# Performance work log

Hardware: AMD Instinct MI355X
Metric: run time of the kernel (lower is better)

The kernel has to match this reference:

```python
import jax, jax.numpy as jnp
import numpy as np

B, T, D, EXP, K = 4, 2048, 1024, 2, 4
H = D * EXP


def setup_inputs() -> dict:
    key = jax.random.key(0)
    ks = jax.random.split(key, 8)
    x = jax.random.normal(ks[0], (B, T, D), jnp.float32)
    W_in = jax.random.normal(ks[1], (2 * H, D), jnp.float32) * D ** -0.5
    s_conv = 1.0 / np.sqrt(K)  # fan_in = (in_ch/groups)*K = K
    W_conv = jax.random.uniform(ks[2], (H, 1, K), jnp.float32, -s_conv, s_conv)
    b_conv = jax.random.uniform(ks[3], (H,), jnp.float32, -s_conv, s_conv)
    W_gates = jax.random.normal(ks[4], (3 * H, H), jnp.float32) * H ** -0.5
    s_g = 1.0 / np.sqrt(H)
    b_gates = jax.random.uniform(ks[5], (3 * H,), jnp.float32, -s_g, s_g)
    W_out = jax.random.normal(ks[6], (D, H), jnp.float32) * H ** -0.5
    alpha_p = jnp.asarray(1.0, jnp.float32)
    return {"x": x, "W_in": W_in, "W_conv": W_conv, "b_conv": b_conv,
            "W_gates": W_gates, "b_gates": b_gates, "W_out": W_out,
            "alpha_p": alpha_p}


def _scan_combine(c1, c2):
    a1, b1 = c1
    a2, b2 = c2
    return (a1 * a2, a2 * b1 + b2)


def reference(x, W_in, W_conv, b_conv, W_gates, b_gates, W_out, alpha_p):
    # input projection -> gate branch and conv branch, each [B,T,H]
    gi = jnp.einsum('btd,ed->bte', x, W_in)
    gate, u = jnp.split(gi, 2, axis=-1)
    # causal depthwise conv over time (torch pads K-1 both sides then keeps [:T])
    uc = jnp.transpose(u, (0, 2, 1))  # [B,H,T]
    v = jax.lax.conv_general_dilated(
        uc, W_conv, window_strides=(1,), padding=[(K - 1, 0)],
        dimension_numbers=('NCH', 'OIH', 'NCH'), feature_group_count=H)
    v = jnp.transpose(v + b_conv[None, :, None], (0, 2, 1))  # [B,T,H]
    # gates
    g = jnp.einsum('bth,gh->btg', v, W_gates) + b_gates
    f, i, o = jnp.split(g, 3, axis=-1)
    # reversed_sigmoid=True: alpha = sigmoid(-f) ** relu(alpha_p)
    alpha = jax.nn.sigmoid(-f) ** jax.nn.relu(alpha_p)
    xin = jax.nn.sigmoid(i) * v
    # diagonal linear recurrence h_t = alpha_t * h_{t-1} + xin_t via parallel scan
    _, h = jax.lax.associative_scan(_scan_combine, (alpha, xin), axis=1)
    h = jax.nn.sigmoid(o) * h
    return jnp.einsum('bth,dh->btd', jax.nn.gelu(gate, approximate=False) * h, W_out)
```

## Files before the change

kernel.cpp:

```cpp
#include <hip/hip_runtime.h>
#include <hip/hip_bf16.h>
#include <cstdint>
#include <cstddef>

#define B_ 4
#define T_ 2048
#define D_ 1024
#define H_ 2048

typedef __attribute__((ext_vector_type(8))) short s8v;
typedef __attribute__((ext_vector_type(4))) float f4v;

__device__ __forceinline__ float bflo(unsigned int u){ union{unsigned int i;float f;}c; c.i=u<<16; return c.f; }
__device__ __forceinline__ float bfhi(unsigned int u){ union{unsigned int i;float f;}c; c.i=u&0xffff0000u; return c.f; }
__device__ __forceinline__ unsigned short f2bf(float f){
    __hip_bfloat16 h = __float2bfloat16(f);
    union { __hip_bfloat16 h; unsigned short u; } c; c.h = h; return c.u;
}
__device__ __forceinline__ unsigned int pk2(float lo, float hi){
    return (unsigned int)f2bf(lo) | ((unsigned int)f2bf(hi) << 16);
}
__device__ __forceinline__ float sigm(float x){ return 1.f/(1.f+expf(-x)); }

__device__ __forceinline__ void gload16(const void* g, void* l){
    __builtin_amdgcn_global_load_lds(
        (const __attribute__((address_space(1))) unsigned int*)g,
        (__attribute__((address_space(3))) unsigned int*)l, 16, 0, 0);
}

__global__ __launch_bounds__(256)
void cvt8(const float* __restrict__ s, unsigned short* __restrict__ d)
{
    size_t i = ((size_t)blockIdx.x*256 + threadIdx.x)*8;
    float4 a = *(const float4*)(s+i), b = *(const float4*)(s+i+4);
    uint4 o; o.x=pk2(a.x,a.y); o.y=pk2(a.z,a.w); o.z=pk2(b.x,b.y); o.w=pk2(b.z,b.w);
    *(uint4*)(d+i)=o;
}

template<int AM, int BM, int EPI>
__global__ __launch_bounds__(256)
void mgemm(const void* __restrict__ Asrc, int lda,
           const void* __restrict__ Bsrc, int K, int N,
           const float* __restrict__ bias,
           unsigned short* __restrict__ C0, unsigned short* __restrict__ C1,
           unsigned short* __restrict__ C2, float* __restrict__ Cf,
           const unsigned short* __restrict__ vsrc, const float* __restrict__ app)
{
    __shared__ unsigned short As[128*64];
    __shared__ unsigned short Bs[128*64];
    const int tid = threadIdx.x;
    const int lane = tid & 63;
    const int wid = tid >> 6;

    const int nwg = gridDim.x * 64;
    const int orig = blockIdx.y * gridDim.x + blockIdx.x;
    const int q = nwg >> 3;
    const int wg = (orig & 7) * q + (orig >> 3);
    const int m0 = (wg & 63) * 128;
    const int n0 = (wg >> 6) * 128;

    const int ar0 = wid * 32;
    const int alr = lane >> 3;
    const int alj = lane & 7;
    const int rr = tid >> 1;
    const int kh = tid & 1;

    const int wm = wid >> 1, wn = wid & 1;
    const int fr = lane & 15, fg = lane >> 4;
    int aoff[4][2], boff[4][2];
#pragma unroll
    for (int m = 0; m < 4; ++m) {
        int row = wm*64 + m*16 + fr;
#pragma unroll
        for (int s = 0; s < 2; ++s)
            aoff[m][s] = row*128 + (((s*4 + fg) ^ (row & 7)) * 16);
    }
#pragma unroll
    for (int n = 0; n < 4; ++n) {
        int row = wn*64 + n*16 + fr;
#pragma unroll
        for (int s = 0; s < 2; ++s)
            boff[n][s] = row*128 + (((s*4 + fg) ^ (row & 7)) * 16);
    }
    const char* Asc = (const char*)As;
    const char* Bsc = (const char*)Bs;

    f4v acc[4][4];
#pragma unroll
    for (int m = 0; m < 4; ++m)
#pragma unroll
        for (int n = 0; n < 4; ++n) { f4v z4 = {0.f,0.f,0.f,0.f}; acc[m][n] = z4; }

    for (int k0 = 0; k0 < K; k0 += 64) {
        if (AM == 1) {
            const unsigned short* Ab = (const unsigned short*)Asrc;
#pragma unroll
            for (int i = 0; i < 4; ++i) {
                int row = ar0 + i*8 + alr;
                int ss = alj ^ alr;
                const char* g = (const char*)(Ab + (size_t)(m0+row)*lda + k0) + ss*16;
                gload16(g, (void*)((char*)As + (ar0 + i*8)*128));
            }
        } else {
            const float* src = (const float*)Asrc + (size_t)(m0+rr)*lda + k0 + kh*32;
            float4 v[8];
#pragma unroll
            for (int i = 0; i < 8; ++i) v[i] = ((const float4*)src)[i];
#pragma unroll
            for (int qd = 0; qd < 4; ++qd) {
                uint4 w;
                w.x = pk2(v[2*qd].x, v[2*qd].y);   w.y = pk2(v[2*qd].z, v[2*qd].w);
                w.z = pk2(v[2*qd+1].x, v[2*qd+1].y); w.w = pk2(v[2*qd+1].z, v[2*qd+1].w);
                int j = (kh*4 + qd) ^ (rr & 7);
                *(uint4*)((char*)As + rr*128 + j*16) = w;
            }
        }
        if (BM == 1) {
            const unsigned short* Bb = (const unsigned short*)Bsrc;
#pragma unroll
            for (int i = 0; i < 4; ++i) {
                int row = ar0 + i*8 + alr;
                int ss = alj ^ alr;
                const char* g = (const char*)(Bb + (size_t)(n0+row)*K + k0) + ss*16;
                gload16(g, (void*)((char*)Bs + (ar0 + i*8)*128));
            }
        } else {
            const float* src = (const float*)Bsrc + (size_t)(n0+rr)*K + k0 + kh*32;
            float4 v[8];
#pragma unroll
            for (int i = 0; i < 8; ++i) v[i] = ((const float4*)src)[i];
#pragma unroll
            for (int qd = 0; qd < 4; ++qd) {
                uint4 w;
                w.x = pk2(v[2*qd].x, v[2*qd].y);   w.y = pk2(v[2*qd].z, v[2*qd].w);
                w.z = pk2(v[2*qd+1].x, v[2*qd+1].y); w.w = pk2(v[2*qd+1].z, v[2*qd+1].w);
                int j = (kh*4 + qd) ^ (rr & 7);
                *(uint4*)((char*)Bs + rr*128 + j*16) = w;
            }
        }
        __syncthreads();
#pragma unroll
        for (int s = 0; s < 2; ++s) {
            s8v a[4], b[4];
#pragma unroll
            for (int m = 0; m < 4; ++m) a[m] = *(const s8v*)(Asc + aoff[m][s]);
#pragma unroll
            for (int n = 0; n < 4; ++n) b[n] = *(const s8v*)(Bsc + boff[n][s]);
#pragma unroll
            for (int m = 0; m < 4; ++m)
#pragma unroll
                for (int n = 0; n < 4; ++n)
                    acc[m][n] = __builtin_amdgcn_mfma_f32_16x16x32_bf16(a[m], b[n], acc[m][n], 0, 0, 0);
        }
        __syncthreads();
    }

    float apv = 1.f; bool ap1 = true;
    if (EPI == 2) { apv = fmaxf(app[0], 0.f); ap1 = (apv == 1.0f); }
    const int cr = (lane >> 4) * 4;
    const int cc = lane & 15;
#pragma unroll
    for (int m = 0; m < 4; ++m) {
        const int grow0 = m0 + wm*64 + m*16 + cr;
#pragma unroll
        for (int n = 0; n < 4; ++n) {
            const int colb = n0 + wn*64 + n*16;
            const int gcol = colb + cc;
            if (EPI == 0) {
#pragma unroll
                for (int j = 0; j < 4; ++j)
                    Cf[(size_t)(grow0+j)*N + gcol] = acc[m][n][j];
            } else if (EPI == 1) {
                unsigned short* dst = (colb < H_) ? C0 : C1;
                const int pc = gcol & (H_-1);
#pragma unroll
                for (int j = 0; j < 4; ++j)
                    dst[(size_t)(grow0+j)*H_ + pc] = f2bf(acc[m][n][j]);
            } else {
                const int plane = colb >> 11;
                const int pc = gcol & (H_-1);
#pragma unroll
                for (int j = 0; j < 4; ++j) {
                    float val = acc[m][n][j] + bias[gcol];
                    const size_t off = (size_t)(grow0+j)*H_ + pc;
                    if (plane == 0) {
                        float s = 1.f/(1.f+expf(val));
                        C0[off] = f2bf(ap1 ? s : powf(s, apv));
                    } else if (plane == 1) {
                        C1[off] = f2bf(sigm(val) * bflo(vsrc[off]));
                    } else {
                        C2[off] = f2bf(sigm(val));
                    }
                }
            }
        }
    }
}

__global__ __launch_bounds__(256)
void conv8(const unsigned short* __restrict__ u, const float* __restrict__ Wc,
           const float* __restrict__ bc, unsigned short* __restrict__ v)
{
    size_t i8 = ((size_t)blockIdx.x*256 + threadIdx.x) * 8;
    int h = (int)(i8 % H_);
    size_t bt = i8 / H_;
    int t = (int)(bt % T_);
    float w[8][4], acc[8];
#pragma unroll
    for (int j = 0; j < 8; ++j) {
        float4 wr = *(const float4*)(Wc + (h+j)*4);
        w[j][0]=wr.x; w[j][1]=wr.y; w[j][2]=wr.z; w[j][3]=wr.w;
        acc[j] = bc[h+j];
    }
    const unsigned short* up = u + bt*H_ + h;
#pragma unroll
    for (int k = 0; k < 4; ++k) {
        int dt = 3 - k;
        if (t >= dt) {
            uint4 r = *(const uint4*)(up - (size_t)dt*H_);
            float e[8] = {bflo(r.x),bfhi(r.x),bflo(r.y),bfhi(r.y),
                          bflo(r.z),bfhi(r.z),bflo(r.w),bfhi(r.w)};
#pragma unroll
            for (int j = 0; j < 8; ++j) acc[j] = fmaf(e[j], w[j][k], acc[j]);
        }
    }
    uint4 o;
    o.x = pk2(acc[0],acc[1]); o.y = pk2(acc[2],acc[3]);
    o.z = pk2(acc[4],acc[5]); o.w = pk2(acc[6],acc[7]);
    *(uint4*)(v + i8) = o;
}

__global__ __launch_bounds__(256)
void scan_chunk8(const unsigned short* __restrict__ al, const unsigned short* __restrict__ xi,
                 float* __restrict__ cA, float* __restrict__ cB, int CT)
{
    int hh = threadIdx.x * 8;
    int c = blockIdx.y, b = blockIdx.z;
    size_t base = ((size_t)b*T_ + (size_t)c*CT)*H_ + hh;
    float A[8], Bv[8];
#pragma unroll
    for (int j=0;j<8;++j){ A[j]=1.f; Bv[j]=0.f; }
    for (int t = 0; t < CT; ++t) {
        uint4 wa = *(const uint4*)(al+base);
        uint4 wx = *(const uint4*)(xi+base);
        float a[8]={bflo(wa.x),bfhi(wa.x),bflo(wa.y),bfhi(wa.y),bflo(wa.z),bfhi(wa.z),bflo(wa.w),bfhi(wa.w)};
        float x[8]={bflo(wx.x),bfhi(wx.x),bflo(wx.y),bfhi(wx.y),bflo(wx.z),bfhi(wx.z),bflo(wx.w),bfhi(wx.w)};
#pragma unroll
        for (int j=0;j<8;++j){ A[j]*=a[j]; Bv[j]=fmaf(a[j],Bv[j],x[j]); }
        base += H_;
    }
    size_t ci = ((size_t)b*gridDim.y + c)*H_ + hh;
    *(float4*)(cA+ci)   = (float4){A[0],A[1],A[2],A[3]};
    *(float4*)(cA+ci+4) = (float4){A[4],A[5],A[6],A[7]};
    *(float4*)(cB+ci)   = (float4){Bv[0],Bv[1],Bv[2],Bv[3]};
    *(float4*)(cB+ci+4) = (float4){Bv[4],Bv[5],Bv[6],Bv[7]};
}

__global__ __launch_bounds__(256)
void scan_carry8(const float* __restrict__ cA, const float* __restrict__ cB,
                 float* __restrict__ cin, int NC)
{
    int gt = blockIdx.x*256 + threadIdx.x;
    int hh = (gt * 8) % H_;
    int b  = (gt * 8) / H_;
    float h[8];
#pragma unroll
    for (int j=0;j<8;++j) h[j]=0.f;
    for (int c = 0; c < NC; ++c) {
        size_t ci = ((size_t)b*NC + c)*H_ + hh;
        *(float4*)(cin+ci)   = (float4){h[0],h[1],h[2],h[3]};
        *(float4*)(cin+ci+4) = (float4){h[4],h[5],h[6],h[7]};
        float4 a0 = *(const float4*)(cA+ci), a1 = *(const float4*)(cA+ci+4);
        float4 b0 = *(const float4*)(cB+ci), b1 = *(const float4*)(cB+ci+4);
        float a[8]={a0.x,a0.y,a0.z,a0.w,a1.x,a1.y,a1.z,a1.w};
        float x[8]={b0.x,b0.y,b0.z,b0.w,b1.x,b1.y,b1.z,b1.w};
#pragma unroll
        for (int j=0;j<8;++j) h[j] = fmaf(a[j], h[j], x[j]);
    }
}

__global__ __launch_bounds__(256)
void scan_apply8(const unsigned short* __restrict__ al, const unsigned short* __restrict__ xi,
                 const unsigned short* __restrict__ so, const unsigned short* __restrict__ ga,
                 const float* __restrict__ cin, unsigned short* __restrict__ z, int CT)
{
    int hh = threadIdx.x * 8;
    int c = blockIdx.y, b = blockIdx.z;
    size_t base = ((size_t)b*T_ + (size_t)c*CT)*H_ + hh;
    size_t ci = ((size_t)b*gridDim.y + c)*H_ + hh;
    float h[8];
    {
        float4 h0 = *(const float4*)(cin+ci), h1 = *(const float4*)(cin+ci+4);
        h[0]=h0.x; h[1]=h0.y; h[2]=h0.z; h[3]=h0.w;
        h[4]=h1.x; h[5]=h1.y; h[6]=h1.z; h[7]=h1.w;
    }
    for (int t = 0; t < CT; ++t) {
        uint4 wa = *(const uint4*)(al+base);
        uint4 wx = *(const uint4*)(xi+base);
        uint4 ws_ = *(const uint4*)(so+base);
        uint4 wg = *(const uint4*)(ga+base);
        float a[8]={bflo(wa.x),bfhi(wa.x),bflo(wa.y),bfhi(wa.y),bflo(wa.z),bfhi(wa.z),bflo(wa.w),bfhi(wa.w)};
        float x[8]={bflo(wx.x),bfhi(wx.x),bflo(wx.y),bfhi(wx.y),bflo(wx.z),bfhi(wx.z),bflo(wx.w),bfhi(wx.w)};
        float s[8]={bflo(ws_.x),bfhi(ws_.x),bflo(ws_.y),bfhi(ws_.y),bflo(ws_.z),bfhi(ws_.z),bflo(ws_.w),bfhi(ws_.w)};
        float g[8]={bflo(wg.x),bfhi(wg.x),bflo(wg.y),bfhi(wg.y),bflo(wg.z),bfhi(wg.z),bflo(wg.w),bfhi(wg.w)};
        float zo[8];
#pragma unroll
        for (int j=0;j<8;++j) {
            h[j] = fmaf(a[j], h[j], x[j]);
            float ge = 0.5f*g[j]*(1.f+erff(g[j]*0.70710678118654752f));
            zo[j] = ge * s[j] * h[j];
        }
        uint4 o;
        o.x = pk2(zo[0],zo[1]); o.y = pk2(zo[2],zo[3]);
        o.z = pk2(zo[4],zo[5]); o.w = pk2(zo[6],zo[7]);
        *(uint4*)(z + base) = o;
        base += H_;
    }
}

__global__ void zero_out(float* __restrict__ out, size_t n)
{
    for (size_t i = (size_t)blockIdx.x*256 + threadIdx.x; i < n; i += (size_t)gridDim.x*256)
        out[i] = 0.f;
}

extern "C" void kernel_launch(void* const* d_in, const int* in_sizes, int n_in,
                              void* d_out, int out_size, void* d_ws, size_t ws_size,
                              hipStream_t stream)
{
    const float* x       = (const float*)d_in[0];
    const float* W_in    = (const float*)d_in[1];
    const float* W_conv  = (const float*)d_in[2];
    const float* b_conv  = (const float*)d_in[3];
    const float* W_gates = (const float*)d_in[4];
    const float* b_gates = (const float*)d_in[5];
    const float* W_out   = (const float*)d_in[6];
    const float* alpha_p = (const float*)d_in[7];
    float* out = (float*)d_out;

    const size_t plane = (size_t)B_ * T_ * H_;
    unsigned short* gate = (unsigned short*)d_ws;
    unsigned short* u    = gate + plane;
    unsigned short* v    = u + plane;
    unsigned short* xin  = v + plane;
    unsigned short* so   = xin + plane;
    char* R = (char*)(so + plane);

    const size_t x_elems  = (size_t)B_*T_*D_;
    const size_t wg_elems = (size_t)3*H_*H_;
    const size_t wi_elems = (size_t)2*H_*D_;
    const size_t wo_elems = (size_t)D_*H_;
    const int NCF = 64;
    const size_t carry_b = 3*(size_t)B_*NCF*H_*4;
    const size_t Rneed = x_elems*2 > carry_b + wo_elems*2 ? x_elems*2 : carry_b + wo_elems*2;
    const size_t need_fast = 5*plane*2 + Rneed;

    if (ws_size >= need_fast && (size_t)out_size*4 >= (wg_elems + wi_elems)*2) {
        unsigned short* wgb  = (unsigned short*)d_out;
        unsigned short* winb = wgb + wg_elems;
        unsigned short* xb   = (unsigned short*)R;
        float* cAp  = (float*)R;
        float* cBp  = cAp + (size_t)B_*NCF*H_;
        float* cinp = cBp + (size_t)B_*NCF*H_;
        unsigned short* woutb = (unsigned short*)(cinp + (size_t)B_*NCF*H_);
        const int CT = T_ / NCF;

        cvt8<<<(unsigned)(x_elems/2048),  256, 0, stream>>>(x, xb);
        cvt8<<<(unsigned)(wi_elems/2048), 256, 0, stream>>>(W_in, winb);
        cvt8<<<(unsigned)(wg_elems/2048), 256, 0, stream>>>(W_gates, wgb);
        mgemm<1,1,1><<<dim3(32,64), 256, 0, stream>>>(
            xb, D_, winb, D_, 2*H_, nullptr, gate, u, nullptr, nullptr, nullptr, nullptr);
        conv8<<<(unsigned)(plane/8/256), 256, 0, stream>>>(u, W_conv, b_conv, v);
        cvt8<<<(unsigned)(wo_elems/2048), 256, 0, stream>>>(W_out, woutb);
        mgemm<1,1,2><<<dim3(48,64), 256, 0, stream>>>(
            v, H_, wgb, H_, 3*H_, b_gates, u, xin, so, nullptr, v, alpha_p);
        scan_chunk8<<<dim3(1,NCF,B_), 256, 0, stream>>>(u, xin, cAp, cBp, CT);
        scan_carry8<<<(B_*H_/8)/256, 256, 0, stream>>>(cAp, cBp, cinp, NCF);
        scan_apply8<<<dim3(1,NCF,B_), 256, 0, stream>>>(u, xin, so, gate, cinp, v, CT);
        mgemm<1,1,0><<<dim3(8,64), 256, 0, stream>>>(
            v, H_, woutb, H_, D_, nullptr, nullptr, nullptr, nullptr, out, nullptr, nullptr);
        return;
    }

    float* cAp = (float*)R;
    int NC = 64;
    if (ws_size < 5*plane*2 + 3*(size_t)B_*64*H_*4) {
        NC = 16;
        if (ws_size < 5*plane*2 + 3*(size_t)B_*16*H_*4) {
            zero_out<<<2048, 256, 0, stream>>>(out, (size_t)out_size);
            return;
        }
    }
    const int CT = T_ / NC;
    float* cBp  = cAp + (size_t)B_*NC*H_;
    float* cinp = cBp + (size_t)B_*NC*H_;

    mgemm<0,0,1><<<dim3(32,64), 256, 0, stream>>>(
        x, D_, W_in, D_, 2*H_, nullptr, gate, u, nullptr, nullptr, nullptr, nullptr);
    conv8<<<(unsigned)(plane/8/256), 256, 0, stream>>>(u, W_conv, b_conv, v);
    mgemm<1,0,2><<<dim3(48,64), 256, 0, stream>>>(
        v, H_, W_gates, H_, 3*H_, b_gates, u, xin, so, nullptr, v, alpha_p);
    scan_chunk8<<<dim3(1,NC,B_), 256, 0, stream>>>(u, xin, cAp, cBp, CT);
    scan_carry8<<<(B_*H_/8)/256, 256, 0, stream>>>(cAp, cBp, cinp, NC);
    scan_apply8<<<dim3(1,NC,B_), 256, 0, stream>>>(u, xin, so, gate, cinp, v, CT);
    mgemm<1,0,0><<<dim3(8,64), 256, 0, stream>>>(
        v, H_, W_out, H_, D_, nullptr, nullptr, nullptr, nullptr, out, nullptr, nullptr);
}
```

Measured before the change: 647.7 us.

## Add 256x256 double-buffered GEMM kernel for input and gate projections

Adds a new GEMM kernel that uses 256x256 output tiles with 512 threads (8 waves, each computing 128x64). It double-buffers LDS and issues the next K-tile's global-to-LDS loads between MFMA phases, raising MFMA priority with s_setprio. The input-projection and gate GEMMs now use it, aiming for more data reuse per loaded byte and overlap of loads with compute. The cost is 128KB of LDS and large accumulator register use, which lowers occupancy, and far fewer workgroups (512 and 768), which may fill the CUs unevenly.

```diff
diff --git a/kernel.cpp b/kernel.cpp
--- a/kernel.cpp
+++ b/kernel.cpp
@@ -37,120 +37,111 @@
     *(uint4*)(d+i)=o;
 }
 
-template<int AM, int BM, int EPI>
-__global__ __launch_bounds__(256)
-void mgemm(const void* __restrict__ Asrc, int lda,
-           const void* __restrict__ Bsrc, int K, int N,
-           const float* __restrict__ bias,
-           unsigned short* __restrict__ C0, unsigned short* __restrict__ C1,
-           unsigned short* __restrict__ C2, float* __restrict__ Cf,
-           const unsigned short* __restrict__ vsrc, const float* __restrict__ app)
-{
-    __shared__ unsigned short As[128*64];
-    __shared__ unsigned short Bs[128*64];
+template<int EPI>
+__global__ __launch_bounds__(512)
+void mgemm256(const unsigned short* __restrict__ A, int lda,
+              const unsigned short* __restrict__ Bw, int K, int N,
+              const float* __restrict__ bias,
+              unsigned short* __restrict__ C0, unsigned short* __restrict__ C1,
+              unsigned short* __restrict__ C2,
+              const unsigned short* __restrict__ vsrc, const float* __restrict__ app)
+{
+    __shared__ unsigned short As[2][256*64];
+    __shared__ unsigned short Bs[2][256*64];
     const int tid = threadIdx.x;
     const int lane = tid & 63;
     const int wid = tid >> 6;
-
-    const int nwg = gridDim.x * 64;
-    const int orig = blockIdx.y * gridDim.x + blockIdx.x;
+    const int wm = wid >> 2;
+    const int wn = wid & 3;
+
+    const int nxb = N >> 8;
+    const int nwg = nxb * 32;
+    const int orig = blockIdx.x;
     const int q = nwg >> 3;
     const int wg = (orig & 7) * q + (orig >> 3);
-    const int m0 = (wg & 63) * 128;
-    const int n0 = (wg >> 6) * 128;
-
-    const int ar0 = wid * 32;
-    const int alr = lane >> 3;
-    const int alj = lane & 7;
-    const int rr = tid >> 1;
-    const int kh = tid & 1;
-
-    const int wm = wid >> 1, wn = wid & 1;
+    const int m0 = (wg & 31) * 256;
+    const int n0 = (wg >> 5) * 256;
+
+    const int srow_in8 = lane >> 3;
+    const int sslot    = (lane & 7) ^ srow_in8;
+    const int NT = K >> 6;
+
     const int fr = lane & 15, fg = lane >> 4;
-    int aoff[4][2], boff[4][2];
-#pragma unroll
-    for (int m = 0; m < 4; ++m) {
-        int row = wm*64 + m*16 + fr;
+    const int sw = fr & 7;
+    int aoff[8][2], boff[4][2];
+#pragma unroll
+    for (int m = 0; m < 8; ++m) {
+        int row = wm*128 + m*16 + fr;
 #pragma unroll
         for (int s = 0; s < 2; ++s)
-            aoff[m][s] = row*128 + (((s*4 + fg) ^ (row & 7)) * 16);
+            aoff[m][s] = row*128 + (((s*4 + fg) ^ sw) * 16);
     }
 #pragma unroll
     for (int n = 0; n < 4; ++n) {
         int row = wn*64 + n*16 + fr;
 #pragma unroll
         for (int s = 0; s < 2; ++s)
-            boff[n][s] = row*128 + (((s*4 + fg) ^ (row & 7)) * 16);
-    }
-    const char* Asc = (const char*)As;
-    const char* Bsc = (const char*)Bs;
-
-    f4v acc[4][4];
-#pragma unroll
-    for (int m = 0; m < 4; ++m)
+            boff[n][s] = row*128 + (((s*4 + fg) ^ sw) * 16);
+    }
+
+    f4v acc[8][4];
+#pragma unroll
+    for (int m = 0; m < 8; ++m)
 #pragma unroll
         for (int n = 0; n < 4; ++n) { f4v z4 = {0.f,0.f,0.f,0.f}; acc[m][n] = z4; }
 
-    for (int k0 = 0; k0 < K; k0 += 64) {
-        if (AM == 1) {
-            const unsigned short* Ab = (const unsigned short*)Asrc;
-#pragma unroll
-            for (int i = 0; i < 4; ++i) {
-                int row = ar0 + i*8 + alr;
-                int ss = alj ^ alr;
-                const char* g = (const char*)(Ab + (size_t)(m0+row)*lda + k0) + ss*16;
-                gload16(g, (void*)((char*)As + (ar0 + i*8)*128));
-            }
-        } else {
-            const float* src = (const float*)Asrc + (size_t)(m0+rr)*lda + k0 + kh*32;
-            float4 v[8];
-#pragma unroll
-            for (int i = 0; i < 8; ++i) v[i] = ((const float4*)src)[i];
-#pragma unroll
-            for (int qd = 0; qd < 4; ++qd) {
-                uint4 w;
-                w.x = pk2(v[2*qd].x, v[2*qd].y);   w.y = pk2(v[2*qd].z, v[2*qd].w);
-                w.z = pk2(v[2*qd+1].x, v[2*qd+1].y); w.w = pk2(v[2*qd+1].z, v[2*qd+1].w);
-                int j = (kh*4 + qd) ^ (rr & 7);
-                *(uint4*)((char*)As + rr*128 + j*16) = w;
-            }
-        }
-        if (BM == 1) {
-            const unsigned short* Bb = (const unsigned short*)Bsrc;
-#pragma unroll
-            for (int i = 0; i < 4; ++i) {
-                int row = ar0 + i*8 + alr;
-                int ss = alj ^ alr;
-                const char* g = (const char*)(Bb + (size_t)(n0+row)*K + k0) + ss*16;
-                gload16(g, (void*)((char*)Bs + (ar0 + i*8)*128));
-            }
-        } else {
-            const float* src = (const float*)Bsrc + (size_t)(n0+rr)*K + k0 + kh*32;
-            float4 v[8];
-#pragma unroll
-            for (int i = 0; i < 8; ++i) v[i] = ((const float4*)src)[i];
-#pragma unroll
-            for (int qd = 0; qd < 4; ++qd) {
-                uint4 w;
-                w.x = pk2(v[2*qd].x, v[2*qd].y);   w.y = pk2(v[2*qd].z, v[2*qd].w);
-                w.z = pk2(v[2*qd+1].x, v[2*qd+1].y); w.w = pk2(v[2*qd+1].z, v[2*qd+1].w);
-                int j = (kh*4 + qd) ^ (rr & 7);
-                *(uint4*)((char*)Bs + rr*128 + j*16) = w;
-            }
-        }
-        __syncthreads();
-#pragma unroll
-        for (int s = 0; s < 2; ++s) {
-            s8v a[4], b[4];
-#pragma unroll
-            for (int m = 0; m < 4; ++m) a[m] = *(const s8v*)(Asc + aoff[m][s]);
-#pragma unroll
-            for (int n = 0; n < 4; ++n) b[n] = *(const s8v*)(Bsc + boff[n][s]);
-#pragma unroll
-            for (int m = 0; m < 4; ++m)
-#pragma unroll
-                for (int n = 0; n < 4; ++n)
-                    acc[m][n] = __builtin_amdgcn_mfma_f32_16x16x32_bf16(a[m], b[n], acc[m][n], 0, 0, 0);
+    auto stageA = [&](int pp, int kt) {
+#pragma unroll
+        for (int c = 0; c < 4; ++c) {
+            int row = c*64 + wid*8 + srow_in8;
+            gload16(A + (size_t)(m0 + row)*lda + kt*64 + sslot*8,
+                    (void*)&As[pp][(c*64 + wid*8) * 64]);
+        }
+    };
+    auto stageB = [&](int pp, int kt) {
+#pragma unroll
+        for (int c = 0; c < 4; ++c) {
+            int row = c*64 + wid*8 + srow_in8;
+            gload16(Bw + (size_t)(n0 + row)*K + kt*64 + sslot*8,
+                    (void*)&Bs[pp][(c*64 + wid*8) * 64]);
+        }
+    };
+
+    stageA(0, 0);
+    stageB(0, 0);
+    __syncthreads();
+
+    for (int t = 0; t < NT; ++t) {
+        const int p = t & 1;
+        const char* Asb = (const char*)&As[p][0];
+        const char* Bsb = (const char*)&Bs[p][0];
+        const bool more = (t + 1 < NT);
+#pragma unroll
+        for (int ph = 0; ph < 4; ++ph) {
+            const int mh = ph >> 1, nh = ph & 1;
+            s8v a[4][2], b[2][2];
+#pragma unroll
+            for (int mi = 0; mi < 4; ++mi)
+#pragma unroll
+                for (int s = 0; s < 2; ++s)
+                    a[mi][s] = *(const s8v*)(Asb + aoff[mh*4 + mi][s]);
+#pragma unroll
+            for (int ni = 0; ni < 2; ++ni)
+#pragma unroll
+                for (int s = 0; s < 2; ++s)
+                    b[ni][s] = *(const s8v*)(Bsb + boff[nh*2 + ni][s]);
+            if (ph == 0 && more) stageA(p ^ 1, t + 1);
+            if (ph == 1 && more) stageB(p ^ 1, t + 1);
+            __builtin_amdgcn_s_setprio(1);
+#pragma unroll
+            for (int mi = 0; mi < 4; ++mi)
+#pragma unroll
+                for (int ni = 0; ni < 2; ++ni)
+#pragma unroll
+                    for (int s = 0; s < 2; ++s)
+                        acc[mh*4+mi][nh*2+ni] = __builtin_amdgcn_mfma_f32_16x16x32_bf16(
+                            a[mi][s], b[ni][s], acc[mh*4+mi][nh*2+ni], 0, 0, 0);
+            __builtin_amdgcn_s_setprio(0);
         }
         __syncthreads();
     }
@@ -160,17 +151,13 @@
     const int cr = (lane >> 4) * 4;
     const int cc = lane & 15;
 #pragma unroll
-    for (int m = 0; m < 4; ++m) {
-        const int grow0 = m0 + wm*64 + m*16 + cr;
+    for (int m = 0; m < 8; ++m) {
+        const int grow0 = m0 + wm*128 + m*16 + cr;
 #pragma unroll
         for (int n = 0; n < 4; ++n) {
             const int colb = n0 + wn*64 + n*16;
             const int gcol = colb + cc;
-            if (EPI == 0) {
-#pragma unroll
-                for (int j = 0; j < 4; ++j)
-                    Cf[(size_t)(grow0+j)*N + gcol] = acc[m][n][j];
-            } else if (EPI == 1) {
+            if (EPI == 1) {
                 unsigned short* dst = (colb < H_) ? C0 : C1;
                 const int pc = gcol & (H_-1);
 #pragma unroll
@@ -197,6 +184,166 @@
     }
 }
 
+template<int AM, int BM, int EPI>
+__global__ __launch_bounds__(256)
+void mgemm(const void* __restrict__ Asrc, int lda,
+           const void* __restrict__ Bsrc, int K, int N,
+           const float* __restrict__ bias,
+           unsigned short* __restrict__ C0, unsigned short* __restrict__ C1,
+           unsigned short* __restrict__ C2, float* __restrict__ Cf,
+           const unsigned short* __restrict__ vsrc, const float* __restrict__ app)
+{
+    __shared__ unsigned short As[128*64];
+    __shared__ unsigned short Bs[128*64];
+    const int tid = threadIdx.x;
+    const int lane = tid & 63;
+    const int wid = tid >> 6;
+
+    const int nwg = gridDim.x * 64;
+    const int orig = blockIdx.y * gridDim.x + blockIdx.x;
+    const int q = nwg >> 3;
+    const int wg = (orig & 7) * q + (orig >> 3);
+    const int m0 = (wg & 63) * 128;
+    const int n0 = (wg >> 6) * 128;
+
+    const int ar0 = wid * 32;
+    const int alr = lane >> 3;
+    const int alj = lane & 7;
+    const int rr = tid >> 1;
+    const int kh = tid & 1;
+
+    const int wm = wid >> 1, wn = wid & 1;
+    const int fr = lane & 15, fg = lane >> 4;
+    int aoff[4][2], boff[4][2];
+#pragma unroll
+    for (int m = 0; m < 4; ++m) {
+        int row = wm*64 + m*16 + fr;
+#pragma unroll
+        for (int s = 0; s < 2; ++s)
+            aoff[m][s] = row*128 + (((s*4 + fg) ^ (row & 7)) * 16);
+    }
+#pragma unroll
+    for (int n = 0; n < 4; ++n) {
+        int row = wn*64 + n*16 + fr;
+#pragma unroll
+        for (int s = 0; s < 2; ++s)
+            boff[n][s] = row*128 + (((s*4 + fg) ^ (row & 7)) * 16);
+    }
+    const char* Asc = (const char*)As;
+    const char* Bsc = (const char*)Bs;
+
+    f4v acc[4][4];
+#pragma unroll
+    for (int m = 0; m < 4; ++m)
+#pragma unroll
+        for (int n = 0; n < 4; ++n) { f4v z4 = {0.f,0.f,0.f,0.f}; acc[m][n] = z4; }
+
+    for (int k0 = 0; k0 < K; k0 += 64) {
+        if (AM == 1) {
+            const unsigned short* Ab = (const unsigned short*)Asrc;
+#pragma unroll
+            for (int i = 0; i < 4; ++i) {
+                int row = ar0 + i*8 + alr;
+                int ss = alj ^ alr;
+                const char* g = (const char*)(Ab + (size_t)(m0+row)*lda + k0) + ss*16;
+                gload16(g, (void*)((char*)As + (ar0 + i*8)*128));
+            }
+        } else {
+            const float* src = (const float*)Asrc + (size_t)(m0+rr)*lda + k0 + kh*32;
+            float4 v[8];
+#pragma unroll
+            for (int i = 0; i < 8; ++i) v[i] = ((const float4*)src)[i];
+#pragma unroll
+            for (int qd = 0; qd < 4; ++qd) {
+                uint4 w;
+                w.x = pk2(v[2*qd].x, v[2*qd].y);   w.y = pk2(v[2*qd].z, v[2*qd].w);
+                w.z = pk2(v[2*qd+1].x, v[2*qd+1].y); w.w = pk2(v[2*qd+1].z, v[2*qd+1].w);
+                int j = (kh*4 + qd) ^ (rr & 7);
+                *(uint4*)((char*)As + rr*128 + j*16) = w;
+            }
+        }
+        if (BM == 1) {
+            const unsigned short* Bb = (const unsigned short*)Bsrc;
+#pragma unroll
+            for (int i = 0; i < 4; ++i) {
+                int row = ar0 + i*8 + alr;
+                int ss = alj ^ alr;
+                const char* g = (const char*)(Bb + (size_t)(n0+row)*K + k0) + ss*16;
+                gload16(g, (void*)((char*)Bs + (ar0 + i*8)*128));
+            }
+        } else {
+            const float* src = (const float*)Bsrc + (size_t)(n0+rr)*K + k0 + kh*32;
+            float4 v[8];
+#pragma unroll
+            for (int i = 0; i < 8; ++i) v[i] = ((const float4*)src)[i];
+#pragma unroll
+            for (int qd = 0; qd < 4; ++qd) {
+                uint4 w;
+                w.x = pk2(v[2*qd].x, v[2*qd].y);   w.y = pk2(v[2*qd].z, v[2*qd].w);
+                w.z = pk2(v[2*qd+1].x, v[2*qd+1].y); w.w = pk2(v[2*qd+1].z, v[2*qd+1].w);
+                int j = (kh*4 + qd) ^ (rr & 7);
+                *(uint4*)((char*)Bs + rr*128 + j*16) = w;
+            }
+        }
+        __syncthreads();
+#pragma unroll
+        for (int s = 0; s < 2; ++s) {
+            s8v a[4], b[4];
+#pragma unroll
+            for (int m = 0; m < 4; ++m) a[m] = *(const s8v*)(Asc + aoff[m][s]);
+#pragma unroll
+            for (int n = 0; n < 4; ++n) b[n] = *(const s8v*)(Bsc + boff[n][s]);
+#pragma unroll
+            for (int m = 0; m < 4; ++m)
+#pragma unroll
+                for (int n = 0; n < 4; ++n)
+                    acc[m][n] = __builtin_amdgcn_mfma_f32_16x16x32_bf16(a[m], b[n], acc[m][n], 0, 0, 0);
+        }
+        __syncthreads();
+    }
+
+    float apv = 1.f; bool ap1 = true;
+    if (EPI == 2) { apv = fmaxf(app[0], 0.f); ap1 = (apv == 1.0f); }
+    const int cr = (lane >> 4) * 4;
+    const int cc = lane & 15;
+#pragma unroll
+    for (int m = 0; m < 4; ++m) {
+        const int grow0 = m0 + wm*64 + m*16 + cr;
+#pragma unroll
+        for (int n = 0; n < 4; ++n) {
+            const int colb = n0 + wn*64 + n*16;
+            const int gcol = colb + cc;
+            if (EPI == 0) {
+#pragma unroll
+                for (int j = 0; j < 4; ++j)
+                    Cf[(size_t)(grow0+j)*N + gcol] = acc[m][n][j];
+            } else if (EPI == 1) {
+                unsigned short* dst = (colb < H_) ? C0 : C1;
+                const int pc = gcol & (H_-1);
+#pragma unroll
+                for (int j = 0; j < 4; ++j)
+                    dst[(size_t)(grow0+j)*H_ + pc] = f2bf(acc[m][n][j]);
+            } else {
+                const int plane = colb >> 11;
+                const int pc = gcol & (H_-1);
+#pragma unroll
+                for (int j = 0; j < 4; ++j) {
+                    float val = acc[m][n][j] + bias[gcol];
+                    const size_t off = (size_t)(grow0+j)*H_ + pc;
+                    if (plane == 0) {
+                        float s = 1.f/(1.f+expf(val));
+                        C0[off] = f2bf(ap1 ? s : powf(s, apv));
+                    } else if (plane == 1) {
+                        C1[off] = f2bf(sigm(val) * bflo(vsrc[off]));
+                    } else {
+                        C2[off] = f2bf(sigm(val));
+                    }
+                }
+            }
+        }
+    }
+}
+
 __global__ __launch_bounds__(256)
 void conv8(const unsigned short* __restrict__ u, const float* __restrict__ Wc,
            const float* __restrict__ bc, unsigned short* __restrict__ v)
@@ -368,12 +515,12 @@
         cvt8<<<(unsigned)(x_elems/2048),  256, 0, stream>>>(x, xb);
         cvt8<<<(unsigned)(wi_elems/2048), 256, 0, stream>>>(W_in, winb);
         cvt8<<<(unsigned)(wg_elems/2048), 256, 0, stream>>>(W_gates, wgb);
-        mgemm<1,1,1><<<dim3(32,64), 256, 0, stream>>>(
-            xb, D_, winb, D_, 2*H_, nullptr, gate, u, nullptr, nullptr, nullptr, nullptr);
+        mgemm256<1><<<dim3(16*32), 512, 0, stream>>>(
+            xb, D_, winb, D_, 2*H_, nullptr, gate, u, nullptr, nullptr, nullptr);
         conv8<<<(unsigned)(plane/8/256), 256, 0, stream>>>(u, W_conv, b_conv, v);
         cvt8<<<(unsigned)(wo_elems/2048), 256, 0, stream>>>(W_out, woutb);
-        mgemm<1,1,2><<<dim3(48,64), 256, 0, stream>>>(
-            v, H_, wgb, H_, 3*H_, b_gates, u, xin, so, nullptr, v, alpha_p);
+        mgemm256<2><<<dim3(24*32), 512, 0, stream>>>(
+            v, H_, wgb, H_, 3*H_, b_gates, u, xin, so, v, alpha_p);
         scan_chunk8<<<dim3(1,NCF,B_), 256, 0, stream>>>(u, xin, cAp, cBp, CT);
         scan_carry8<<<(B_*H_/8)/256, 256, 0, stream>>>(cAp, cBp, cinp, NCF);
         scan_apply8<<<dim3(1,NCF,B_), 256, 0, stream>>>(u, xin, so, gate, cinp, v, CT);
```

Result: no change. 643.3 us (-0.7%).
